# Kernel tuning notes

Measured on AMD Instinct MI355X. Metric: run time of the kernel, lower is better.

## Reference

```python
import jax, jax.numpy as jnp
import numpy as np

EPS = 1e-7  # K.epsilon()
NUM_CAPS = 2
N_IN = 17 * 21 * 16 * 16  # 91392
DIM_IN = 8
DIM_OUT = 16
ROUTINGS = 3


def squash(s):
    sn = jnp.sum(jnp.square(s), axis=-1, keepdims=True)
    return sn / (1.0 + sn) / jnp.sqrt(sn + EPS) * s


def setup_inputs() -> dict:
    key = jax.random.key(0)
    k1, k2 = jax.random.split(key)
    B = 16
    x = jax.random.normal(k1, (B, N_IN, DIM_IN), dtype=jnp.float32)
    # glorot_uniform for W [2, N_IN, 8, 16]
    limit = np.sqrt(6.0 / (DIM_IN + DIM_OUT))
    W = jax.random.uniform(k2, (NUM_CAPS, N_IN, DIM_IN, DIM_OUT), dtype=jnp.float32,
                           minval=-limit, maxval=limit)
    return {"x": x, "W": W}


def reference(x, W):
    # u_hat[b,j,n,o] = sum_i x[b,n,i] * W[j,n,i,o]
    u_hat = jnp.einsum('bni,jnio->bjno', x, W)  # [B,2,N,16]
    B = x.shape[0]
    b = jnp.zeros((B, NUM_CAPS, N_IN), dtype=x.dtype)
    v = None
    for it in range(ROUTINGS):
        c = jax.nn.softmax(b, axis=1)                    # over output capsules
        s = jnp.einsum('bjn,bjno->bjo', c, u_hat)        # [B,2,16]
        v = squash(s)
        if it < ROUTINGS - 1:
            b = b + jnp.einsum('bjo,bjno->bjn', v, u_hat)
    return v
```

## Files before the change

kernel.cpp:

```cpp
#include <hip/hip_runtime.h>
#include <math.h>

#define NIN 91392
#define DIN 8
#define DOUT 16
#define NCHUNK (NIN / 8)
#define GRID_P 768
#define TPB 512

typedef float f32x4 __attribute__((ext_vector_type(4)));

#define GLD_LDS16(gp, lp) __builtin_amdgcn_global_load_lds(                    \
    (const __attribute__((address_space(1))) float*)(gp),                      \
    (__attribute__((address_space(3))) float*)(lp), 16, 0, 0)

#define DSR128(dst, pf)                                                        \
    asm volatile("ds_read_b128 %0, %1" : "=v"(dst)                             \
        : "v"((unsigned)(__SIZE_TYPE__)                                        \
              (const __attribute__((address_space(3))) float*)(pf)))

__device__ __forceinline__ void issue_round(
    const float* __restrict__ x, const float* __restrict__ W,
    float* lds, int bid, int grid, int k, int lane, int wave)
{
    const int wR_half = lane >> 5;
    const int wFlo = (lane & 31) * 4;
    const int xb = (wave & 3) * 4 + (lane >> 4);
    const int xu = (lane & 15) ^ (xb & 7);
    const int xs = wave >> 2;
    const int bufb = k & 1;
    {   const int m = 2*wave; const int s = m>>3, p = m&7;
        int c_ = bid + (2*k + s) * grid; if (c_ >= NCHUNK) c_ = bid;
        const int R = 2*p + wR_half;
        GLD_LDS16(W + (size_t)(R>>3)*((size_t)NIN*128)
                    + (size_t)(c_*8 + (R&7))*128 + wFlo,
                  lds + bufb*4096 + s*2048 + p*256);
    }
    {   const int m = 2*wave+1; const int s = m>>3, p = m&7;
        int c_ = bid + (2*k + s) * grid; if (c_ >= NCHUNK) c_ = bid;
        const int R = 2*p + wR_half;
        GLD_LDS16(W + (size_t)(R>>3)*((size_t)NIN*128)
                    + (size_t)(c_*8 + (R&7))*128 + wFlo,
                  lds + bufb*4096 + s*2048 + p*256);
    }
    {   int c_ = bid + (2*k + xs) * grid; if (c_ >= NCHUNK) c_ = bid;
        GLD_LDS16(x + (size_t)xb*((size_t)NIN*8) + (size_t)c_*64 + xu*4,
                  lds + 8192 + bufb*2048 + xs*1024 + (wave&3)*256);
    }
}

template<int PASS>
__global__ __launch_bounds__(TPB) void caps_pass(
    const float* __restrict__ x, const float* __restrict__ W,
    const float* __restrict__ vin, float* __restrict__ part, int grid)
{
    const int t = threadIdx.x;
    const int lane = t & 63;
    const int wave = t >> 6;
    const int og = lane & 3;
    const int j  = (lane >> 2) & 1;
    const int b0 = lane >> 3;
    const int bid = blockIdx.x;

    __shared__ __align__(16) float lds[12288];

    const float sgn = j ? -1.f : 1.f;

    f32x4 vinA = {0.f,0.f,0.f,0.f}, vinB = {0.f,0.f,0.f,0.f};
    if (PASS > 0) {
        vinA = sgn * *(const f32x4*)(vin + b0 * 32 + j * 16 + og * 4);
        vinB = sgn * *(const f32x4*)(vin + (b0 + 8) * 32 + j * 16 + og * 4);
    }

    f32x4 accA = {0.f,0.f,0.f,0.f};
    f32x4 accB = {0.f,0.f,0.f,0.f};

    const int R_rounds = (NCHUNK + 2*grid - 1) / (2*grid);

    issue_round(x, W, lds, bid, grid, 0, lane, wave);
    issue_round(x, W, lds, bid, grid, 1, lane, wave);

    for (int k = 0; k < R_rounds; ++k) {
        asm volatile("s_waitcnt vmcnt(3)" ::: "memory");
        __builtin_amdgcn_s_barrier();

        const int bufb = k & 1;
        #pragma unroll
        for (int s = 0; s < 2; ++s) {
            const int c = bid + (2*k + s) * grid;
            if (c < NCHUNK) {
                const float* wrow = lds + bufb*4096 + s*2048
                                  + (j*8 + wave)*128 + og*4;
                const float* xrg  = lds + 8192 + bufb*2048 + s*1024;
                const int u0i = wave * 2;
                const int swz = (b0 & 7);

                f32x4 u0 = {0.f,0.f,0.f,0.f};
                f32x4 u1 = {0.f,0.f,0.f,0.f};
                {
                    f32x4 W0,W1,W2,W3,XA,XB;
                    DSR128(W0, wrow + 0);
                    DSR128(W1, wrow + 16);
                    DSR128(W2, wrow + 32);
                    DSR128(W3, wrow + 48);
                    DSR128(XA, xrg + b0*64     + ((u0i^swz) << 2));
                    DSR128(XB, xrg + (b0+8)*64 + ((u0i^swz) << 2));
                    asm volatile("s_waitcnt lgkmcnt(0)");
                    __builtin_amdgcn_sched_barrier(0);
                    u0 += W0*XA.x; u0 += W1*XA.y; u0 += W2*XA.z; u0 += W3*XA.w;
                    u1 += W0*XB.x; u1 += W1*XB.y; u1 += W2*XB.z; u1 += W3*XB.w;
                }
                {
                    f32x4 W4,W5,W6,W7,XC,XD;
                    DSR128(W4, wrow + 64);
                    DSR128(W5, wrow + 80);
                    DSR128(W6, wrow + 96);
                    DSR128(W7, wrow + 112);
                    DSR128(XC, xrg + b0*64     + (((u0i+1)^swz) << 2));
                    DSR128(XD, xrg + (b0+8)*64 + (((u0i+1)^swz) << 2));
                    asm volatile("s_waitcnt lgkmcnt(0)");
                    __builtin_amdgcn_sched_barrier(0);
                    u0 += W4*XC.x; u0 += W5*XC.y; u0 += W6*XC.z; u0 += W7*XC.w;
                    u1 += W4*XD.x; u1 += W5*XD.y; u1 += W6*XD.z; u1 += W7*XD.w;
                }

                if (PASS == 0) {
                    accA += u0;
                    accB += u1;
                } else {
                    float m0 = vinA.x*u0.x + vinA.y*u0.y + vinA.z*u0.z + vinA.w*u0.w;
                    float m1 = vinB.x*u1.x + vinB.y*u1.y + vinB.z*u1.z + vinB.w*u1.w;
                    m0 += __shfl_xor(m0, 1);  m1 += __shfl_xor(m1, 1);
                    m0 += __shfl_xor(m0, 2);  m1 += __shfl_xor(m1, 2);
                    m0 += __shfl_xor(m0, 4);  m1 += __shfl_xor(m1, 4);
                    const float cA = __builtin_amdgcn_rcpf(1.f + __expf(-sgn * m0));
                    const float cB = __builtin_amdgcn_rcpf(1.f + __expf(-sgn * m1));
                    accA += u0 * cA;
                    accB += u1 * cB;
                }
            }
        }
        asm volatile("s_waitcnt lgkmcnt(0)" ::: "memory");
        __builtin_amdgcn_s_barrier();
        issue_round(x, W, lds, bid, grid, k + 2, lane, wave);
    }

    asm volatile("s_waitcnt vmcnt(0)" ::: "memory");
    __syncthreads();

    {
        float* sl = lds + wave * 576 + lane * 9;
        sl[0]=accA.x; sl[1]=accA.y; sl[2]=accA.z; sl[3]=accA.w;
        sl[4]=accB.x; sl[5]=accB.y; sl[6]=accB.z; sl[7]=accB.w;
    }
    __syncthreads();
    if (t < 64) {
        float s[8];
        #pragma unroll
        for (int q = 0; q < 8; ++q) s[q] = 0.f;
        #pragma unroll
        for (int w = 0; w < 8; ++w) {
            const float* p = lds + w * 576 + t * 9;
            #pragma unroll
            for (int q = 0; q < 8; ++q) s[q] += p[q];
        }
        const int tb0 = t >> 3, tj = (t >> 2) & 1, tog = t & 3;
        #pragma unroll
        for (int q = 0; q < 4; ++q) {
            part[(size_t)(tb0*32 + tj*16 + tog*4 + q) * grid + bid] = s[q];
            part[(size_t)((tb0+8)*32 + tj*16 + tog*4 + q) * grid + bid] = s[4+q];
        }
    }
}

template<int PASS>
__global__ __launch_bounds__(256) void caps_reduce(
    const float* __restrict__ part, const float* __restrict__ vprev,
    float* __restrict__ vout, int gridA)
{
    const int blk = blockIdx.x;
    const int b = blk >> 1, j = blk & 1;
    const int t = threadIdx.x;
    const int o = t & 15;
    const int ch = t >> 4;
    const size_t base = ((size_t)b * 32 + j * 16 + o) * gridA;
    float s = 0.f;
    for (int g = ch; g < gridA; g += 16) s += part[base + g];
    __shared__ float red[256];
    red[t] = s;
    __syncthreads();
    if (t < 16) {
        float sv = 0.f;
        #pragma unroll
        for (int c = 0; c < 16; ++c) sv += red[c * 16 + t];
        if (PASS == 0) sv *= 0.5f;
        float sq = sv * sv;
        sq += __shfl_xor(sq, 1);
        sq += __shfl_xor(sq, 2);
        sq += __shfl_xor(sq, 4);
        sq += __shfl_xor(sq, 8);
        const float sn = sq;
        float v = sv * sn / ((1.f + sn) * sqrtf(sn + 1e-7f));
        if (PASS == 1) v += vprev[b * 32 + j * 16 + o];
        vout[b * 32 + j * 16 + o] = v;
    }
}

extern "C" void kernel_launch(void* const* d_in, const int* in_sizes, int n_in,
                              void* d_out, int out_size, void* d_ws, size_t ws_size,
                              hipStream_t stream) {
    const float* x = (const float*)d_in[0];
    const float* W = (const float*)d_in[1];
    float* out = (float*)d_out;

    size_t maxg = (ws_size - 4096) / (512 * sizeof(float));
    int GRID = (int)(maxg < GRID_P ? maxg : GRID_P);
    if (GRID < 1) GRID = 1;

    float* part = (float*)d_ws;
    float* v0   = part + (size_t)512 * GRID;
    float* vsum = v0 + 512;

    caps_pass<0><<<GRID, TPB, 0, stream>>>(x, W, nullptr, part, GRID);
    caps_reduce<0><<<32, 256, 0, stream>>>(part, nullptr, v0, GRID);
    caps_pass<1><<<GRID, TPB, 0, stream>>>(x, W, v0, part, GRID);
    caps_reduce<1><<<32, 256, 0, stream>>>(part, v0, vsum, GRID);
    caps_pass<2><<<GRID, TPB, 0, stream>>>(x, W, vsum, part, GRID);
    caps_reduce<2><<<32, 256, 0, stream>>>(part, nullptr, out, GRID);
}
```

Before: 129.9 us.

## Fuse three routing passes and reductions into one cooperative kernel

Replaces the six separate launches (three streaming passes plus three small reductions) with a single cooperative kernel that uses grid-wide syncs between each pass and an in-kernel reduction done by 32 blocks. The goal is to remove per-launch overhead and the idle tail between dependent kernels. In exchange it adds grid barriers, a threadfence, and a grid size capped by occupancy, which could limit parallelism. The old multi-launch path stays as a fallback if the cooperative launch fails.

```diff
diff --git a/kernel.cpp b/kernel.cpp
--- a/kernel.cpp
+++ b/kernel.cpp
@@ -1,5 +1,8 @@
 #include <hip/hip_runtime.h>
+#include <hip/hip_cooperative_groups.h>
 #include <math.h>
+
+namespace cg = cooperative_groups;
 
 #define NIN 91392
 #define DIN 8
@@ -50,28 +53,12 @@
 }
 
 template<int PASS>
-__global__ __launch_bounds__(TPB) void caps_pass(
+__device__ __forceinline__ void pass_core(
     const float* __restrict__ x, const float* __restrict__ W,
-    const float* __restrict__ vin, float* __restrict__ part, int grid)
-{
-    const int t = threadIdx.x;
-    const int lane = t & 63;
-    const int wave = t >> 6;
-    const int og = lane & 3;
-    const int j  = (lane >> 2) & 1;
-    const int b0 = lane >> 3;
-    const int bid = blockIdx.x;
-
-    __shared__ __align__(16) float lds[12288];
-
-    const float sgn = j ? -1.f : 1.f;
-
-    f32x4 vinA = {0.f,0.f,0.f,0.f}, vinB = {0.f,0.f,0.f,0.f};
-    if (PASS > 0) {
-        vinA = sgn * *(const f32x4*)(vin + b0 * 32 + j * 16 + og * 4);
-        vinB = sgn * *(const f32x4*)(vin + (b0 + 8) * 32 + j * 16 + og * 4);
-    }
-
+    float* part, float* lds, int bid, int grid,
+    int t, int lane, int wave, int og, int j, int b0,
+    f32x4 vinA, f32x4 vinB, float sgn)
+{
     f32x4 accA = {0.f,0.f,0.f,0.f};
     f32x4 accB = {0.f,0.f,0.f,0.f};
 
@@ -174,6 +161,32 @@
 }
 
 template<int PASS>
+__global__ __launch_bounds__(TPB) void caps_pass(
+    const float* __restrict__ x, const float* __restrict__ W,
+    const float* __restrict__ vin, float* __restrict__ part, int grid)
+{
+    const int t = threadIdx.x;
+    const int lane = t & 63;
+    const int wave = t >> 6;
+    const int og = lane & 3;
+    const int j  = (lane >> 2) & 1;
+    const int b0 = lane >> 3;
+    const int bid = blockIdx.x;
+
+    __shared__ __align__(16) float lds[12288];
+
+    const float sgn = j ? -1.f : 1.f;
+
+    f32x4 vinA = {0.f,0.f,0.f,0.f}, vinB = {0.f,0.f,0.f,0.f};
+    if (PASS > 0) {
+        vinA = sgn * *(const f32x4*)(vin + b0 * 32 + j * 16 + og * 4);
+        vinB = sgn * *(const f32x4*)(vin + (b0 + 8) * 32 + j * 16 + og * 4);
+    }
+    pass_core<PASS>(x, W, part, lds, bid, grid, t, lane, wave, og, j, b0,
+                    vinA, vinB, sgn);
+}
+
+template<int PASS>
 __global__ __launch_bounds__(256) void caps_reduce(
     const float* __restrict__ part, const float* __restrict__ vprev,
     float* __restrict__ vout, int gridA)
@@ -206,6 +219,79 @@
     }
 }
 
+__global__ __launch_bounds__(TPB) void caps_fused(
+    const float* __restrict__ x, const float* __restrict__ W,
+    float* part, float* vwork, float* out)
+{
+    const int t = threadIdx.x;
+    const int lane = t & 63;
+    const int wave = t >> 6;
+    const int og = lane & 3;
+    const int j  = (lane >> 2) & 1;
+    const int b0 = lane >> 3;
+    const int bid = blockIdx.x;
+    const int grid = gridDim.x;
+
+    __shared__ __align__(16) float lds[12288];
+
+    const float sgn = j ? -1.f : 1.f;
+    float v0keep = 0.f;
+
+    cg::grid_group gg = cg::this_grid();
+
+    for (int p = 0; p < 3; ++p) {
+        f32x4 vinA = {0.f,0.f,0.f,0.f}, vinB = {0.f,0.f,0.f,0.f};
+        if (p > 0) {
+            vinA = sgn * *(const f32x4*)(vwork + b0 * 32 + j * 16 + og * 4);
+            vinB = sgn * *(const f32x4*)(vwork + (b0 + 8) * 32 + j * 16 + og * 4);
+        }
+
+        if (p == 0)
+            pass_core<0>(x, W, part, lds, bid, grid, t, lane, wave, og, j, b0,
+                         vinA, vinB, sgn);
+        else
+            pass_core<1>(x, W, part, lds, bid, grid, t, lane, wave, og, j, b0,
+                         vinA, vinB, sgn);
+
+        __threadfence();
+        gg.sync();
+
+        if (bid < 32) {
+            const int rb = bid >> 1, rj = bid & 1;
+            float s = 0.f;
+            if (t < 256) {
+                const int o = t & 15, ch = t >> 4;
+                const size_t base = ((size_t)rb * 32 + rj * 16 + o) * grid;
+                for (int g2 = ch; g2 < grid; g2 += 16) s += part[base + g2];
+            }
+            __syncthreads();
+            if (t < 256) lds[t] = s;
+            __syncthreads();
+            if (t < 16) {
+                float sv = 0.f;
+                #pragma unroll
+                for (int c = 0; c < 16; ++c) sv += lds[c * 16 + t];
+                if (p == 0) sv *= 0.5f;
+                float sq = sv * sv;
+                sq += __shfl_xor(sq, 1);
+                sq += __shfl_xor(sq, 2);
+                sq += __shfl_xor(sq, 4);
+                sq += __shfl_xor(sq, 8);
+                const float sn = sq;
+                float v = sv * sn / ((1.f + sn) * sqrtf(sn + 1e-7f));
+                const int idx = rb * 32 + rj * 16 + t;
+                if (p == 0)      { v0keep = v;  vwork[idx] = v; }
+                else if (p == 1) {              vwork[idx] = v0keep + v; }
+                else             {              out[idx]   = v; }
+            }
+            __syncthreads();
+        }
+
+        __threadfence();
+        if (p < 2) gg.sync();
+    }
+}
+
 extern "C" void kernel_launch(void* const* d_in, const int* in_sizes, int n_in,
                               void* d_out, int out_size, void* d_ws, size_t ws_size,
                               hipStream_t stream) {
@@ -213,18 +299,35 @@
     const float* W = (const float*)d_in[1];
     float* out = (float*)d_out;
 
-    size_t maxg = (ws_size - 4096) / (512 * sizeof(float));
+    size_t maxg = (ws_size - 8192) / (512 * sizeof(float));
     int GRID = (int)(maxg < GRID_P ? maxg : GRID_P);
-    if (GRID < 1) GRID = 1;
+    if (GRID < 32) GRID = 32;
 
     float* part = (float*)d_ws;
-    float* v0   = part + (size_t)512 * GRID;
-    float* vsum = v0 + 512;
-
-    caps_pass<0><<<GRID, TPB, 0, stream>>>(x, W, nullptr, part, GRID);
-    caps_reduce<0><<<32, 256, 0, stream>>>(part, nullptr, v0, GRID);
-    caps_pass<1><<<GRID, TPB, 0, stream>>>(x, W, v0, part, GRID);
-    caps_reduce<1><<<32, 256, 0, stream>>>(part, v0, vsum, GRID);
-    caps_pass<2><<<GRID, TPB, 0, stream>>>(x, W, vsum, part, GRID);
-    caps_reduce<2><<<32, 256, 0, stream>>>(part, nullptr, out, GRID);
-}
+    float* vbuf = part + (size_t)512 * GRID;
+    float* vsum = vbuf + 512;
+
+    int mbpc = 0;
+    hipError_t qerr = hipOccupancyMaxActiveBlocksPerMultiprocessor(
+        &mbpc, (const void*)caps_fused, TPB, 0);
+    int coopGrid = GRID;
+    if (qerr == hipSuccess && mbpc > 0) {
+        int cap = mbpc * 256;
+        if (coopGrid > cap) coopGrid = cap;
+    }
+    if (coopGrid < 32) coopGrid = 32;
+
+    void* kargs[] = {(void*)&x, (void*)&W, (void*)&part, (void*)&vbuf,
+                     (void*)&out};
+    hipError_t lerr = hipLaunchCooperativeKernel(
+        (void*)caps_fused, dim3(coopGrid), dim3(TPB), kargs, 0, stream);
+
+    if (lerr != hipSuccess) {
+        caps_pass<0><<<GRID, TPB, 0, stream>>>(x, W, nullptr, part, GRID);
+        caps_reduce<0><<<32, 256, 0, stream>>>(part, nullptr, vbuf, GRID);
+        caps_pass<1><<<GRID, TPB, 0, stream>>>(x, W, vbuf, part, GRID);
+        caps_reduce<1><<<32, 256, 0, stream>>>(part, vbuf, vsum, GRID);
+        caps_pass<2><<<GRID, TPB, 0, stream>>>(x, W, vsum, part, GRID);
+        caps_reduce<2><<<32, 256, 0, stream>>>(part, nullptr, out, GRID);
+    }
+}
```

Result: slower. 486.0 us (+274.1%).
